# Performance work log

Measured on AMD Instinct MI355X. Metric: run time of the kernel, lower is better.

## Reference

```python
import jax, jax.numpy as jnp
import numpy as np

# E8P 12-bit-abs codebook construction (faithful vectorized port of the torch code)
_SHUF = np.array([0, 2, 1, 3, 4, 6, 5, 7])  # shuffle_map
# get_norm12() * 2 (the integer matrix before the /2)
_NORM12_X2 = np.array([
    [3, 1, 1, 1, 3, 3, 3, 3], [1, 3, 1, 1, 3, 3, 3, 3], [1, 1, 3, 1, 3, 3, 3, 3],
    [1, 1, 1, 3, 3, 3, 3, 3], [3, 3, 3, 1, 3, 3, 1, 1], [3, 3, 3, 1, 3, 1, 3, 1],
    [3, 3, 3, 1, 1, 3, 3, 1], [3, 3, 3, 1, 3, 1, 1, 3], [3, 3, 3, 1, 1, 3, 1, 3],
    [3, 3, 3, 1, 1, 1, 3, 3], [3, 3, 1, 3, 3, 3, 1, 1], [3, 3, 1, 3, 3, 1, 3, 1],
    [3, 3, 1, 3, 1, 3, 3, 1], [3, 3, 1, 3, 3, 1, 1, 3], [3, 3, 1, 3, 1, 3, 1, 3],
    [3, 3, 1, 3, 1, 1, 3, 3], [3, 1, 3, 3, 3, 3, 1, 1], [3, 1, 3, 3, 3, 1, 3, 1],
    [3, 1, 3, 3, 1, 3, 3, 1], [3, 1, 3, 3, 3, 1, 1, 3], [3, 1, 3, 3, 1, 3, 1, 3],
    [1, 3, 3, 3, 1, 1, 3, 3], [1, 3, 3, 3, 3, 3, 1, 1], [1, 3, 3, 3, 3, 1, 3, 1],
    [1, 3, 3, 3, 1, 3, 3, 1], [1, 3, 3, 3, 3, 1, 1, 3], [1, 3, 3, 3, 1, 3, 1, 3],
    [1, 1, 3, 3, 1, 3, 3, 3], [3, 3, 1, 1, 3, 3, 3, 1]], dtype=np.int64)


def _packed_abs_grid():
    # Enumerate D8+1/2 lattice points, working with doubled integer coords (odd ints in [-7,7])
    idx = np.arange(8 ** 8, dtype=np.int64)
    cols, s, nrm = [], 0, 0
    for i in range(8):  # torch.cartesian_prod order: first dim varies slowest
        v = (2 * (((idx >> (3 * (7 - i))) & 7) - 4) + 1).astype(np.int8)  # 2*x for x in {-3.5..3.5}
        cols.append(v)
        w = v.astype(np.int32)
        s = s + w
        nrm = nrm + w * w
    mask = (s % 4 == 0) & (nrm <= 40)
    V = np.stack([c[mask] for c in cols], axis=1)
    d8abs2 = np.unique(np.abs(V), axis=0).astype(np.int64)  # lexsorted, doubled abs values
    cba2 = np.concatenate([d8abs2, _NORM12_X2], axis=0)[:, _SHUF]  # doubled values (== 2*cba)
    parity = (cba2.sum(1) // 2) % 2  # == cba.sum(1) % 2
    col = cba2 * 2  # == cba * 4, integer byte values in [2,14]
    col[:, 7] = col[:, 7] * (1 - 2 * parity)
    acc = np.zeros(col.shape[0], dtype=np.int64)
    for i in range(8):
        acc = acc | (col[:, i] << (8 * i))
    assert acc.shape[0] == 256
    return acc


def _full_grid():
    # Decode all 2^16 codes into the [65536, 8] fp32 codebook (port of get_full_grid)
    acc = _packed_abs_grid()
    c = np.arange(1 << 16, dtype=np.int64)
    signs = c & 255
    p = signs ^ (signs >> 4)
    p ^= p >> 2
    p ^= p >> 1
    parity = p & 1  # xor of the 8 sign bits
    signs = signs ^ parity
    ac = acc[c >> 8]  # packed abs code per entry
    byt = ((ac[:, None] >> (8 * _SHUF)) & 255).astype(np.uint8).astype(np.int8).astype(np.float32) / 4.0
    neg = ((signs[:, None] >> (7 - _SHUF)) & 1).astype(bool)
    vals = np.where(neg, -byt, byt) + np.where(parity[:, None] == 1, np.float32(-0.25), np.float32(0.25))
    return vals.astype(np.float32)


def setup_inputs() -> dict:
    key = jax.random.key(0)
    k1, k2 = jax.random.split(key)
    B = 4096          # tokens (batch * seq)
    M = 4096          # out_features = Qidxs rows
    N = 512           # Qidxs cols; in_features = N * 8 = 4096
    inp = jax.random.normal(k1, (B, N * 8), dtype=jnp.float32)
    Qidxs = jax.random.randint(k2, (M, N), 0, 1 << 16, dtype=jnp.int32)
    grid = jnp.asarray(_full_grid())  # [65536, 8] fp32 decoded E8P codebook
    return {"input": inp, "Qidxs": Qidxs, "grid": grid}


def reference(input, Qidxs, grid):
    m, n = Qidxs.shape
    # Dequantize: each int16 code indexes an 8-vector of the E8P codebook
    W = jnp.take(grid, Qidxs, axis=0).reshape(m, n * 8)  # [m, n*8] decompressed weight
    return input @ W.T  # [B, m]
```

## Files before the change

### kernel.cpp

```cpp
#include <hip/hip_runtime.h>
#include <hip/hip_bf16.h>

#define B_DIM 4096
#define M_DIM 4096
#define K_DIM 4096
#define NCODE 512

typedef __attribute__((ext_vector_type(4))) float f32x4;
typedef __attribute__((ext_vector_type(8))) short short8;

__device__ __forceinline__ unsigned short f2bf(float f) {
    union { float f; unsigned u; } c; c.f = f;
    unsigned u = c.u;
    return (unsigned short)((u + 0x7FFFu + ((u >> 16) & 1u)) >> 16);
}

__global__ __launch_bounds__(256) void prep_kernel(const int* __restrict__ Q,
                                                   const float* __restrict__ cb,
                                                   short* __restrict__ Wout,
                                                   const float* __restrict__ in,
                                                   short* __restrict__ Ab) {
    const int b = blockIdx.x;
    if (b < 8192) {
        const int t = b * 256 + threadIdx.x;
        const int code = Q[t] & 0xFFFF;
        const float4* g = (const float4*)(cb + (size_t)code * 8);
        const float4 v0 = g[0];
        const float4 v1 = g[1];
        short8 o;
        o[0] = f2bf(v0.x); o[1] = f2bf(v0.y); o[2] = f2bf(v0.z); o[3] = f2bf(v0.w);
        o[4] = f2bf(v1.x); o[5] = f2bf(v1.y); o[6] = f2bf(v1.z); o[7] = f2bf(v1.w);
        *(short8*)(Wout + (size_t)t * 8) = o;
    } else {
        const int t = (b - 8192) * 256 + threadIdx.x;
        const float4* p = (const float4*)(in + (size_t)t * 8);
        const float4 v0 = p[0];
        const float4 v1 = p[1];
        short8 o;
        o[0] = f2bf(v0.x); o[1] = f2bf(v0.y); o[2] = f2bf(v0.z); o[3] = f2bf(v0.w);
        o[4] = f2bf(v1.x); o[5] = f2bf(v1.y); o[6] = f2bf(v1.z); o[7] = f2bf(v1.w);
        *(short8*)(Ab + (size_t)t * 8) = o;
    }
}

#define BM 256
#define BN 256
#define BK 64
#define NT (K_DIM / BK)

#define GLD(src, dst) \
    __builtin_amdgcn_global_load_lds( \
        (const __attribute__((address_space(1))) void*)(src), \
        (__attribute__((address_space(3))) void*)(dst), 16, 0, 0)

#define MFMA(a, b, c) __builtin_amdgcn_mfma_f32_16x16x32_bf16(a, b, c, 0, 0, 0)

__global__ __launch_bounds__(512, 2) void gemm_bt_kernel(const short* __restrict__ A,
                                                         const short* __restrict__ Wd,
                                                         float* __restrict__ C) {
    __shared__ short lds[2 * 32768];

    const int tid  = threadIdx.x;
    const int wave = tid >> 6;
    const int lane = tid & 63;

    const int bid = blockIdx.x;
    const int xcd = bid & 7;
    const int s   = bid >> 3;
    const int by  = (xcd >> 1) * 4 + (s >> 3);
    const int bx  = (xcd & 1) * 8 + (s & 7);

    const int rowBase = by * BM;
    const int colBase = bx * BN;

    const int wr = wave >> 2;
    const int wc = wave & 3;

    const int rA0 = tid >> 3;
    const int uu  = (tid & 7) ^ (rA0 & 7);
    const int stOff = rA0 * 64 + (tid & 7) * 8;
    const short* aSrcB = A  + (size_t)(rowBase + rA0) * K_DIM + uu * 8;
    const short* bSrcB = Wd + (size_t)(colBase + rA0) * K_DIM + uu * 8;

    const int l15 = lane & 15;
    const int l4  = lane >> 4;
    const int uk0 = ((l4 ^ (l15 & 7))) * 8;
    const int uk1 = uk0 ^ 32;
    const int aRow = (wr * 128 + l15) * 64;
    const int bRow = 16384 + (wc * 64 + l15) * 64;

    f32x4 acc[8][4] = {};
    short8 aC[4], bC[4];

#pragma unroll
    for (int c = 0; c < 4; ++c)
        GLD(aSrcB + c * (64 * K_DIM), &lds[c * 4096 + stOff]);
#pragma unroll
    for (int c = 0; c < 4; ++c)
        GLD(bSrcB + c * (64 * K_DIM), &lds[16384 + c * 4096 + stOff]);
    asm volatile("s_waitcnt vmcnt(0)" ::: "memory");
    __builtin_amdgcn_s_barrier();
#pragma unroll
    for (int m = 0; m < 4; ++m) aC[m] = *(const short8*)&lds[aRow + m * 1024 + uk0];
#pragma unroll
    for (int n = 0; n < 4; ++n) bC[n] = *(const short8*)&lds[bRow + n * 1024 + uk0];

    for (int t = 0; t < NT; ++t) {
        const int buf  = (t & 1) * 32768;
        const int bufn = buf ^ 32768;
        const size_t kpre = (size_t)(((t + 1 < NT) ? (t + 1) : (NT - 1)) * BK);

        short8 a1h0[4];
#pragma unroll
        for (int m = 0; m < 4; ++m)
            a1h0[m] = *(const short8*)&lds[buf + aRow + (m + 4) * 1024 + uk0];
#pragma unroll
        for (int c = 0; c < 4; ++c)
            GLD(aSrcB + kpre + c * (64 * K_DIM), &lds[bufn + c * 4096 + stOff]);
        __builtin_amdgcn_s_setprio(1);
#pragma unroll
        for (int m = 0; m < 4; ++m)
#pragma unroll
            for (int n = 0; n < 4; ++n)
                acc[m][n] = MFMA(aC[m], bC[n], acc[m][n]);
        __builtin_amdgcn_s_setprio(0);

        short8 a0h1[4], b1[4];
#pragma unroll
        for (int m = 0; m < 4; ++m)
            a0h1[m] = *(const short8*)&lds[buf + aRow + m * 1024 + uk1];
#pragma unroll
        for (int n = 0; n < 4; ++n)
            b1[n] = *(const short8*)&lds[buf + bRow + n * 1024 + uk1];
#pragma unroll
        for (int c = 0; c < 4; ++c)
            GLD(bSrcB + kpre + c * (64 * K_DIM), &lds[bufn + 16384 + c * 4096 + stOff]);
        __builtin_amdgcn_s_setprio(1);
#pragma unroll
        for (int m = 0; m < 4; ++m)
#pragma unroll
            for (int n = 0; n < 4; ++n)
                acc[m + 4][n] = MFMA(a1h0[m], bC[n], acc[m + 4][n]);
        __builtin_amdgcn_s_setprio(0);

        short8 a1h1[4];
#pragma unroll
        for (int m = 0; m < 4; ++m)
            a1h1[m] = *(const short8*)&lds[buf + aRow + (m + 4) * 1024 + uk1];
        __builtin_amdgcn_s_setprio(1);
#pragma unroll
        for (int m = 0; m < 4; ++m)
#pragma unroll
            for (int n = 0; n < 4; ++n)
                acc[m][n] = MFMA(a0h1[m], b1[n], acc[m][n]);
        __builtin_amdgcn_s_setprio(0);
        asm volatile("s_waitcnt vmcnt(0)" ::: "memory");
        __builtin_amdgcn_s_barrier();

#pragma unroll
        for (int m = 0; m < 4; ++m)
            aC[m] = *(const short8*)&lds[bufn + aRow + m * 1024 + uk0];
#pragma unroll
        for (int n = 0; n < 4; ++n)
            bC[n] = *(const short8*)&lds[bufn + bRow + n * 1024 + uk0];
        __builtin_amdgcn_s_setprio(1);
#pragma unroll
        for (int m = 0; m < 4; ++m)
#pragma unroll
            for (int n = 0; n < 4; ++n)
                acc[m + 4][n] = MFMA(a1h1[m], b1[n], acc[m + 4][n]);
        __builtin_amdgcn_s_setprio(0);
        asm volatile("s_waitcnt lgkmcnt(8)" ::: "memory");
        __builtin_amdgcn_s_barrier();
    }

    const int r0 = rowBase + wr * 128 + l4 * 4;
    const int c0 = colBase + wc * 64 + l15;
#pragma unroll
    for (int m = 0; m < 8; ++m)
#pragma unroll
        for (int n = 0; n < 4; ++n) {
            float* cp = C + (size_t)(r0 + m * 16) * M_DIM + (c0 + n * 16);
#pragma unroll
            for (int reg = 0; reg < 4; ++reg)
                cp[(size_t)reg * M_DIM] = acc[m][n][reg];
        }
}

extern "C" void kernel_launch(void* const* d_in, const int* in_sizes, int n_in,
                              void* d_out, int out_size, void* d_ws, size_t ws_size,
                              hipStream_t stream) {
    const float* inp  = (const float*)d_in[0];
    const int*   qidx = (const int*)d_in[1];
    const float* cb   = (const float*)d_in[2];
    float* out = (float*)d_out;

    short* Wb = (short*)d_ws;
    short* Ab = Wb + (size_t)M_DIM * K_DIM;

    prep_kernel<<<16384, 256, 0, stream>>>(qidx, cb, Wb, inp, Ab);

    gemm_bt_kernel<<<256, 512, 0, stream>>>(Ab, Wb, out);
}
```

Baseline: 133.4 us.

## Fuse fp32-to-bf16 input conversion into GEMM A-tile loads

Drops the separate input conversion pass in the prep kernel. The GEMM now loads fp32 activations straight into registers, converts them to bf16 and writes them to LDS itself, in place of the direct global-to-LDS loads. This removes a 64MB fp32 read plus a 32MB bf16 write and reread of the activation matrix. In exchange the GEMM reads A as fp32 (twice the bytes, and each tile is reread by 16 column blocks), uses more registers, and adds conversion ALU work and an lgkmcnt(0) wait inside the main loop.

```diff
diff --git a/kernel.cpp b/kernel.cpp
--- a/kernel.cpp
+++ b/kernel.cpp
@@ -17,30 +17,16 @@
 
 __global__ __launch_bounds__(256) void prep_kernel(const int* __restrict__ Q,
                                                    const float* __restrict__ cb,
-                                                   short* __restrict__ Wout,
-                                                   const float* __restrict__ in,
-                                                   short* __restrict__ Ab) {
-    const int b = blockIdx.x;
-    if (b < 8192) {
-        const int t = b * 256 + threadIdx.x;
-        const int code = Q[t] & 0xFFFF;
-        const float4* g = (const float4*)(cb + (size_t)code * 8);
-        const float4 v0 = g[0];
-        const float4 v1 = g[1];
-        short8 o;
-        o[0] = f2bf(v0.x); o[1] = f2bf(v0.y); o[2] = f2bf(v0.z); o[3] = f2bf(v0.w);
-        o[4] = f2bf(v1.x); o[5] = f2bf(v1.y); o[6] = f2bf(v1.z); o[7] = f2bf(v1.w);
-        *(short8*)(Wout + (size_t)t * 8) = o;
-    } else {
-        const int t = (b - 8192) * 256 + threadIdx.x;
-        const float4* p = (const float4*)(in + (size_t)t * 8);
-        const float4 v0 = p[0];
-        const float4 v1 = p[1];
-        short8 o;
-        o[0] = f2bf(v0.x); o[1] = f2bf(v0.y); o[2] = f2bf(v0.z); o[3] = f2bf(v0.w);
-        o[4] = f2bf(v1.x); o[5] = f2bf(v1.y); o[6] = f2bf(v1.z); o[7] = f2bf(v1.w);
-        *(short8*)(Ab + (size_t)t * 8) = o;
-    }
+                                                   short* __restrict__ Wout) {
+    const int t = blockIdx.x * 256 + threadIdx.x;
+    const int code = Q[t] & 0xFFFF;
+    const float4* g = (const float4*)(cb + (size_t)code * 8);
+    const float4 v0 = g[0];
+    const float4 v1 = g[1];
+    short8 o;
+    o[0] = f2bf(v0.x); o[1] = f2bf(v0.y); o[2] = f2bf(v0.z); o[3] = f2bf(v0.w);
+    o[4] = f2bf(v1.x); o[5] = f2bf(v1.y); o[6] = f2bf(v1.z); o[7] = f2bf(v1.w);
+    *(short8*)(Wout + (size_t)t * 8) = o;
 }
 
 #define BM 256
@@ -55,7 +41,7 @@
 
 #define MFMA(a, b, c) __builtin_amdgcn_mfma_f32_16x16x32_bf16(a, b, c, 0, 0, 0)
 
-__global__ __launch_bounds__(512, 2) void gemm_bt_kernel(const short* __restrict__ A,
+__global__ __launch_bounds__(512, 2) void gemm_bt_kernel(const float* __restrict__ Af,
                                                          const short* __restrict__ Wd,
                                                          float* __restrict__ C) {
     __shared__ short lds[2 * 32768];
@@ -79,7 +65,7 @@
     const int rA0 = tid >> 3;
     const int uu  = (tid & 7) ^ (rA0 & 7);
     const int stOff = rA0 * 64 + (tid & 7) * 8;
-    const short* aSrcB = A  + (size_t)(rowBase + rA0) * K_DIM + uu * 8;
+    const float* aSrcF = Af + (size_t)(rowBase + rA0) * K_DIM + uu * 8;
     const short* bSrcB = Wd + (size_t)(colBase + rA0) * K_DIM + uu * 8;
 
     const int l15 = lane & 15;
@@ -91,14 +77,28 @@
 
     f32x4 acc[8][4] = {};
     short8 aC[4], bC[4];
-
-#pragma unroll
-    for (int c = 0; c < 4; ++c)
-        GLD(aSrcB + c * (64 * K_DIM), &lds[c * 4096 + stOff]);
+    float4 fa[4][2];
+
+#pragma unroll
+    for (int c = 0; c < 4; ++c) {
+        const float4* p = (const float4*)(aSrcF + (size_t)c * (64 * K_DIM));
+        fa[c][0] = p[0];
+        fa[c][1] = p[1];
+    }
 #pragma unroll
     for (int c = 0; c < 4; ++c)
         GLD(bSrcB + c * (64 * K_DIM), &lds[16384 + c * 4096 + stOff]);
+#pragma unroll
+    for (int c = 0; c < 4; ++c) {
+        short8 w;
+        w[0] = f2bf(fa[c][0].x); w[1] = f2bf(fa[c][0].y);
+        w[2] = f2bf(fa[c][0].z); w[3] = f2bf(fa[c][0].w);
+        w[4] = f2bf(fa[c][1].x); w[5] = f2bf(fa[c][1].y);
+        w[6] = f2bf(fa[c][1].z); w[7] = f2bf(fa[c][1].w);
+        *(short8*)&lds[c * 4096 + stOff] = w;
+    }
     asm volatile("s_waitcnt vmcnt(0)" ::: "memory");
+    asm volatile("s_waitcnt lgkmcnt(0)" ::: "memory");
     __builtin_amdgcn_s_barrier();
 #pragma unroll
     for (int m = 0; m < 4; ++m) aC[m] = *(const short8*)&lds[aRow + m * 1024 + uk0];
@@ -115,8 +115,11 @@
         for (int m = 0; m < 4; ++m)
             a1h0[m] = *(const short8*)&lds[buf + aRow + (m + 4) * 1024 + uk0];
 #pragma unroll
-        for (int c = 0; c < 4; ++c)
-            GLD(aSrcB + kpre + c * (64 * K_DIM), &lds[bufn + c * 4096 + stOff]);
+        for (int c = 0; c < 4; ++c) {
+            const float4* p = (const float4*)(aSrcF + kpre + (size_t)c * (64 * K_DIM));
+            fa[c][0] = p[0];
+            fa[c][1] = p[1];
+        }
         __builtin_amdgcn_s_setprio(1);
 #pragma unroll
         for (int m = 0; m < 4; ++m)
@@ -147,6 +150,15 @@
 #pragma unroll
         for (int m = 0; m < 4; ++m)
             a1h1[m] = *(const short8*)&lds[buf + aRow + (m + 4) * 1024 + uk1];
+#pragma unroll
+        for (int c = 0; c < 4; ++c) {
+            short8 w;
+            w[0] = f2bf(fa[c][0].x); w[1] = f2bf(fa[c][0].y);
+            w[2] = f2bf(fa[c][0].z); w[3] = f2bf(fa[c][0].w);
+            w[4] = f2bf(fa[c][1].x); w[5] = f2bf(fa[c][1].y);
+            w[6] = f2bf(fa[c][1].z); w[7] = f2bf(fa[c][1].w);
+            *(short8*)&lds[bufn + c * 4096 + stOff] = w;
+        }
         __builtin_amdgcn_s_setprio(1);
 #pragma unroll
         for (int m = 0; m < 4; ++m)
@@ -155,6 +167,7 @@
                 acc[m][n] = MFMA(a0h1[m], b1[n], acc[m][n]);
         __builtin_amdgcn_s_setprio(0);
         asm volatile("s_waitcnt vmcnt(0)" ::: "memory");
+        asm volatile("s_waitcnt lgkmcnt(0)" ::: "memory");
         __builtin_amdgcn_s_barrier();
 
 #pragma unroll
@@ -196,9 +209,9 @@
     float* out = (float*)d_out;
 
     short* Wb = (short*)d_ws;
-    short* Ab = Wb + (size_t)M_DIM * K_DIM;
-
-    prep_kernel<<<16384, 256, 0, stream>>>(qidx, cb, Wb, inp, Ab);
-
-    gemm_bt_kernel<<<256, 512, 0, stream>>>(Ab, Wb, out);
-}
+
+    const int n_codes = M_DIM * NCODE;
+    prep_kernel<<<n_codes / 256, 256, 0, stream>>>(qidx, cb, Wb);
+
+    gemm_bt_kernel<<<256, 512, 0, stream>>>(inp, Wb, out);
+}
```

Result: slower. 166.5 us (+24.8%).

## Triple-buffer B tile in LDS to prefetch two K-steps ahead

Applied to the files above, without the earlier changes.

Splits LDS into separate A (double) and B (triple) buffers and issues B global-to-LDS loads two iterations ahead, waiting with vmcnt(4) instead of draining all loads. The aim is to hide global load latency for the weight tile behind more MFMA work. LDS use grows from 128KB to 160KB per block, which with launch bounds of 2 blocks per CU may exceed LDS capacity and lower occupancy.

```diff
diff --git a/kernel.cpp b/kernel.cpp
--- a/kernel.cpp
+++ b/kernel.cpp
@@ -48,6 +48,9 @@
 #define BK 64
 #define NT (K_DIM / BK)
 
+#define ABUF(i) ((i) * 16384)
+#define BBUF(i) (32768 + (i) * 16384)
+
 #define GLD(src, dst) \
     __builtin_amdgcn_global_load_lds( \
         (const __attribute__((address_space(1))) void*)(src), \
@@ -58,7 +61,7 @@
 __global__ __launch_bounds__(512, 2) void gemm_bt_kernel(const short* __restrict__ A,
                                                          const short* __restrict__ Wd,
                                                          float* __restrict__ C) {
-    __shared__ short lds[2 * 32768];
+    __shared__ short lds[81920];
 
     const int tid  = threadIdx.x;
     const int wave = tid >> 6;
@@ -87,36 +90,47 @@
     const int uk0 = ((l4 ^ (l15 & 7))) * 8;
     const int uk1 = uk0 ^ 32;
     const int aRow = (wr * 128 + l15) * 64;
-    const int bRow = 16384 + (wc * 64 + l15) * 64;
+    const int bRow = (wc * 64 + l15) * 64;
 
     f32x4 acc[8][4] = {};
     short8 aC[4], bC[4];
 
 #pragma unroll
     for (int c = 0; c < 4; ++c)
-        GLD(aSrcB + c * (64 * K_DIM), &lds[c * 4096 + stOff]);
+        GLD(aSrcB + c * (64 * K_DIM), &lds[ABUF(0) + c * 4096 + stOff]);
 #pragma unroll
     for (int c = 0; c < 4; ++c)
-        GLD(bSrcB + c * (64 * K_DIM), &lds[16384 + c * 4096 + stOff]);
-    asm volatile("s_waitcnt vmcnt(0)" ::: "memory");
+        GLD(bSrcB + c * (64 * K_DIM), &lds[BBUF(0) + c * 4096 + stOff]);
+#pragma unroll
+    for (int c = 0; c < 4; ++c)
+        GLD(bSrcB + BK + c * (64 * K_DIM), &lds[BBUF(1) + c * 4096 + stOff]);
+    asm volatile("s_waitcnt vmcnt(4)" ::: "memory");
     __builtin_amdgcn_s_barrier();
 #pragma unroll
-    for (int m = 0; m < 4; ++m) aC[m] = *(const short8*)&lds[aRow + m * 1024 + uk0];
-#pragma unroll
-    for (int n = 0; n < 4; ++n) bC[n] = *(const short8*)&lds[bRow + n * 1024 + uk0];
-
+    for (int m = 0; m < 4; ++m)
+        aC[m] = *(const short8*)&lds[ABUF(0) + aRow + m * 1024 + uk0];
+#pragma unroll
+    for (int n = 0; n < 4; ++n)
+        bC[n] = *(const short8*)&lds[BBUF(0) + bRow + n * 1024 + uk0];
+
+    int bcur = 0;
     for (int t = 0; t < NT; ++t) {
-        const int buf  = (t & 1) * 32768;
-        const int bufn = buf ^ 32768;
-        const size_t kpre = (size_t)(((t + 1 < NT) ? (t + 1) : (NT - 1)) * BK);
+        const int abuf  = ABUF(t & 1);
+        const int abufn = ABUF((t + 1) & 1);
+        const int bbuf  = BBUF(bcur);
+        const int bnx1  = (bcur + 1 < 3) ? (bcur + 1) : 0;
+        const int bnx2  = (bnx1 + 1 < 3) ? (bnx1 + 1) : 0;
+        const int bbufn = BBUF(bnx1);
+        const size_t kpre1 = (size_t)(((t + 1 < NT) ? (t + 1) : (NT - 1)) * BK);
+        const size_t kpre2 = (size_t)(((t + 2 < NT) ? (t + 2) : (NT - 1)) * BK);
 
         short8 a1h0[4];
 #pragma unroll
         for (int m = 0; m < 4; ++m)
-            a1h0[m] = *(const short8*)&lds[buf + aRow + (m + 4) * 1024 + uk0];
+            a1h0[m] = *(const short8*)&lds[abuf + aRow + (m + 4) * 1024 + uk0];
 #pragma unroll
         for (int c = 0; c < 4; ++c)
-            GLD(aSrcB + kpre + c * (64 * K_DIM), &lds[bufn + c * 4096 + stOff]);
+            GLD(aSrcB + kpre1 + c * (64 * K_DIM), &lds[abufn + c * 4096 + stOff]);
         __builtin_amdgcn_s_setprio(1);
 #pragma unroll
         for (int m = 0; m < 4; ++m)
@@ -128,13 +142,14 @@
         short8 a0h1[4], b1[4];
 #pragma unroll
         for (int m = 0; m < 4; ++m)
-            a0h1[m] = *(const short8*)&lds[buf + aRow + m * 1024 + uk1];
+            a0h1[m] = *(const short8*)&lds[abuf + aRow + m * 1024 + uk1];
 #pragma unroll
         for (int n = 0; n < 4; ++n)
-            b1[n] = *(const short8*)&lds[buf + bRow + n * 1024 + uk1];
+            b1[n] = *(const short8*)&lds[bbuf + bRow + n * 1024 + uk1];
 #pragma unroll
         for (int c = 0; c < 4; ++c)
-            GLD(bSrcB + kpre + c * (64 * K_DIM), &lds[bufn + 16384 + c * 4096 + stOff]);
+            GLD(bSrcB + kpre2 + c * (64 * K_DIM),
+                &lds[BBUF(bnx2) + c * 4096 + stOff]);
         __builtin_amdgcn_s_setprio(1);
 #pragma unroll
         for (int m = 0; m < 4; ++m)
@@ -146,7 +161,7 @@
         short8 a1h1[4];
 #pragma unroll
         for (int m = 0; m < 4; ++m)
-            a1h1[m] = *(const short8*)&lds[buf + aRow + (m + 4) * 1024 + uk1];
+            a1h1[m] = *(const short8*)&lds[abuf + aRow + (m + 4) * 1024 + uk1];
         __builtin_amdgcn_s_setprio(1);
 #pragma unroll
         for (int m = 0; m < 4; ++m)
@@ -154,15 +169,15 @@
             for (int n = 0; n < 4; ++n)
                 acc[m][n] = MFMA(a0h1[m], b1[n], acc[m][n]);
         __builtin_amdgcn_s_setprio(0);
-        asm volatile("s_waitcnt vmcnt(0)" ::: "memory");
+        asm volatile("s_waitcnt vmcnt(4)" ::: "memory");
         __builtin_amdgcn_s_barrier();
 
 #pragma unroll
         for (int m = 0; m < 4; ++m)
-            aC[m] = *(const short8*)&lds[bufn + aRow + m * 1024 + uk0];
+            aC[m] = *(const short8*)&lds[abufn + aRow + m * 1024 + uk0];
 #pragma unroll
         for (int n = 0; n < 4; ++n)
-            bC[n] = *(const short8*)&lds[bufn + bRow + n * 1024 + uk0];
+            bC[n] = *(const short8*)&lds[bbufn + bRow + n * 1024 + uk0];
         __builtin_amdgcn_s_setprio(1);
 #pragma unroll
         for (int m = 0; m < 4; ++m)
@@ -172,6 +187,8 @@
         __builtin_amdgcn_s_setprio(0);
         asm volatile("s_waitcnt lgkmcnt(8)" ::: "memory");
         __builtin_amdgcn_s_barrier();
+
+        bcur = bnx1;
     }
 
     const int r0 = rowBase + wr * 128 + l4 * 4;
```

Result: no change. 135.8 us (+1.8%).

## Restructure GEMM main loop into 8-wave ping-pong schedule with staggered A/B prefetch

Applied to the files above, without the earlier changes.

Rewrites the bf16 GEMM inner loop into four MFMA phases, each separated by barriers. Each phase loads a subset of fragments and issues one half of the next tile's global-to-LDS loads. B is prefetched two tiles ahead into the buffer currently being consumed, while A is prefetched one tile ahead, so loads are spread across the iteration. The goal is better overlap of LDS reads and global loads with MFMA work, at the cost of more barriers and more complex buffer-hazard reasoning.

```diff
diff --git a/kernel.cpp b/kernel.cpp
--- a/kernel.cpp
+++ b/kernel.cpp
@@ -82,6 +82,15 @@
     const short* aSrcB = A  + (size_t)(rowBase + rA0) * K_DIM + uu * 8;
     const short* bSrcB = Wd + (size_t)(colBase + rA0) * K_DIM + uu * 8;
 
+#define STAGE_A(tt, h, dstbuf) { \
+        const size_t ko = (size_t)(tt) * BK; \
+        GLD(aSrcB + ko + (2*(h))   * (64 * K_DIM), &lds[(dstbuf) + (2*(h))   * 4096 + stOff]); \
+        GLD(aSrcB + ko + (2*(h)+1) * (64 * K_DIM), &lds[(dstbuf) + (2*(h)+1) * 4096 + stOff]); }
+#define STAGE_B(tt, h, dstbuf) { \
+        const size_t ko = (size_t)(tt) * BK; \
+        GLD(bSrcB + ko + (2*(h))   * (64 * K_DIM), &lds[(dstbuf) + 16384 + (2*(h))   * 4096 + stOff]); \
+        GLD(bSrcB + ko + (2*(h)+1) * (64 * K_DIM), &lds[(dstbuf) + 16384 + (2*(h)+1) * 4096 + stOff]); }
+
     const int l15 = lane & 15;
     const int l4  = lane >> 4;
     const int uk0 = ((l4 ^ (l15 & 7))) * 8;
@@ -90,87 +99,80 @@
     const int bRow = 16384 + (wc * 64 + l15) * 64;
 
     f32x4 acc[8][4] = {};
-    short8 aC[4], bC[4];
-
-#pragma unroll
-    for (int c = 0; c < 4; ++c)
-        GLD(aSrcB + c * (64 * K_DIM), &lds[c * 4096 + stOff]);
-#pragma unroll
-    for (int c = 0; c < 4; ++c)
-        GLD(bSrcB + c * (64 * K_DIM), &lds[16384 + c * 4096 + stOff]);
-    asm volatile("s_waitcnt vmcnt(0)" ::: "memory");
+
+    STAGE_A(0, 0, 0); STAGE_A(0, 1, 0);
+    STAGE_B(0, 0, 0); STAGE_B(0, 1, 0);
+    STAGE_B(1, 0, 32768); STAGE_B(1, 1, 32768);
+    asm volatile("s_waitcnt vmcnt(4)" ::: "memory");
     __builtin_amdgcn_s_barrier();
-#pragma unroll
-    for (int m = 0; m < 4; ++m) aC[m] = *(const short8*)&lds[aRow + m * 1024 + uk0];
-#pragma unroll
-    for (int n = 0; n < 4; ++n) bC[n] = *(const short8*)&lds[bRow + n * 1024 + uk0];
 
     for (int t = 0; t < NT; ++t) {
         const int buf  = (t & 1) * 32768;
-        const int bufn = buf ^ 32768;
-        const size_t kpre = (size_t)(((t + 1 < NT) ? (t + 1) : (NT - 1)) * BK);
-
-        short8 a1h0[4];
-#pragma unroll
-        for (int m = 0; m < 4; ++m)
-            a1h0[m] = *(const short8*)&lds[buf + aRow + (m + 4) * 1024 + uk0];
-#pragma unroll
-        for (int c = 0; c < 4; ++c)
-            GLD(aSrcB + kpre + c * (64 * K_DIM), &lds[bufn + c * 4096 + stOff]);
-        __builtin_amdgcn_s_setprio(1);
-#pragma unroll
-        for (int m = 0; m < 4; ++m)
-#pragma unroll
-            for (int n = 0; n < 4; ++n)
-                acc[m][n] = MFMA(aC[m], bC[n], acc[m][n]);
-        __builtin_amdgcn_s_setprio(0);
-
-        short8 a0h1[4], b1[4];
-#pragma unroll
-        for (int m = 0; m < 4; ++m)
-            a0h1[m] = *(const short8*)&lds[buf + aRow + m * 1024 + uk1];
+        const int bufo = buf ^ 32768;
+        const int t1c  = (t + 1 < NT) ? (t + 1) : (NT - 1);
+        const int t2c  = (t + 2 < NT) ? (t + 2) : (NT - 1);
+
+        short8 aF[8], b01[2], b23[2], bk1[4];
+
+#pragma unroll
+        for (int m = 0; m < 8; ++m)
+            aF[m] = *(const short8*)&lds[buf + aRow + m * 1024 + uk0];
+        b01[0] = *(const short8*)&lds[buf + bRow + 0    + uk0];
+        b01[1] = *(const short8*)&lds[buf + bRow + 1024 + uk0];
+        STAGE_A(t1c, 0, bufo);
+        __builtin_amdgcn_s_barrier();
+        asm volatile("s_waitcnt lgkmcnt(0)" ::: "memory");
+        __builtin_amdgcn_s_setprio(1);
+#pragma unroll
+        for (int m = 0; m < 8; ++m)
+#pragma unroll
+            for (int n = 0; n < 2; ++n)
+                acc[m][n] = MFMA(aF[m], b01[n], acc[m][n]);
+        __builtin_amdgcn_s_setprio(0);
+        __builtin_amdgcn_s_barrier();
+
+        b23[0] = *(const short8*)&lds[buf + bRow + 2048 + uk0];
+        b23[1] = *(const short8*)&lds[buf + bRow + 3072 + uk0];
 #pragma unroll
         for (int n = 0; n < 4; ++n)
-            b1[n] = *(const short8*)&lds[buf + bRow + n * 1024 + uk1];
-#pragma unroll
-        for (int c = 0; c < 4; ++c)
-            GLD(bSrcB + kpre + c * (64 * K_DIM), &lds[bufn + 16384 + c * 4096 + stOff]);
-        __builtin_amdgcn_s_setprio(1);
-#pragma unroll
-        for (int m = 0; m < 4; ++m)
-#pragma unroll
-            for (int n = 0; n < 4; ++n)
-                acc[m + 4][n] = MFMA(a1h0[m], bC[n], acc[m + 4][n]);
-        __builtin_amdgcn_s_setprio(0);
-
-        short8 a1h1[4];
-#pragma unroll
-        for (int m = 0; m < 4; ++m)
-            a1h1[m] = *(const short8*)&lds[buf + aRow + (m + 4) * 1024 + uk1];
-        __builtin_amdgcn_s_setprio(1);
-#pragma unroll
-        for (int m = 0; m < 4; ++m)
-#pragma unroll
-            for (int n = 0; n < 4; ++n)
-                acc[m][n] = MFMA(a0h1[m], b1[n], acc[m][n]);
-        __builtin_amdgcn_s_setprio(0);
-        asm volatile("s_waitcnt vmcnt(0)" ::: "memory");
-        __builtin_amdgcn_s_barrier();
-
-#pragma unroll
-        for (int m = 0; m < 4; ++m)
-            aC[m] = *(const short8*)&lds[bufn + aRow + m * 1024 + uk0];
-#pragma unroll
-        for (int n = 0; n < 4; ++n)
-            bC[n] = *(const short8*)&lds[bufn + bRow + n * 1024 + uk0];
-        __builtin_amdgcn_s_setprio(1);
-#pragma unroll
-        for (int m = 0; m < 4; ++m)
-#pragma unroll
-            for (int n = 0; n < 4; ++n)
-                acc[m + 4][n] = MFMA(a1h1[m], b1[n], acc[m + 4][n]);
-        __builtin_amdgcn_s_setprio(0);
-        asm volatile("s_waitcnt lgkmcnt(8)" ::: "memory");
+            bk1[n] = *(const short8*)&lds[buf + bRow + n * 1024 + uk1];
+        STAGE_A(t1c, 1, bufo);
+        __builtin_amdgcn_s_barrier();
+        asm volatile("s_waitcnt lgkmcnt(0)" ::: "memory");
+        __builtin_amdgcn_s_setprio(1);
+#pragma unroll
+        for (int m = 0; m < 8; ++m)
+#pragma unroll
+            for (int n = 0; n < 2; ++n)
+                acc[m][n + 2] = MFMA(aF[m], b23[n], acc[m][n + 2]);
+        __builtin_amdgcn_s_setprio(0);
+        __builtin_amdgcn_s_barrier();
+
+#pragma unroll
+        for (int m = 0; m < 8; ++m)
+            aF[m] = *(const short8*)&lds[buf + aRow + m * 1024 + uk1];
+        STAGE_B(t2c, 0, buf);
+        __builtin_amdgcn_s_barrier();
+        asm volatile("s_waitcnt lgkmcnt(0)" ::: "memory");
+        __builtin_amdgcn_s_setprio(1);
+#pragma unroll
+        for (int m = 0; m < 8; ++m)
+#pragma unroll
+            for (int n = 0; n < 2; ++n)
+                acc[m][n] = MFMA(aF[m], bk1[n], acc[m][n]);
+        __builtin_amdgcn_s_setprio(0);
+        __builtin_amdgcn_s_barrier();
+
+        STAGE_B(t2c, 1, buf);
+        asm volatile("s_waitcnt vmcnt(4)" ::: "memory");
+        __builtin_amdgcn_s_barrier();
+        __builtin_amdgcn_s_setprio(1);
+#pragma unroll
+        for (int m = 0; m < 8; ++m)
+#pragma unroll
+            for (int n = 0; n < 2; ++n)
+                acc[m][n + 2] = MFMA(aF[m], bk1[n + 2], acc[m][n + 2]);
+        __builtin_amdgcn_s_setprio(0);
         __builtin_amdgcn_s_barrier();
     }
 
```

After: 140.7 us. 5.5% more time.
